# Optimization experiments

Measured on AMD Instinct MI355X. Metric: run time of the kernel, lower is better.

## Reference

```python
import jax, jax.numpy as jnp
import numpy as np

B, T, C = 64, 256, 1024
H, DH = 16, 64           # n_heads, head_dim (C == H*DH)
NP, WS = 16, 2           # n_patches per side, window_size (T == NP*NP)
EPS = 1e-5


def setup_inputs() -> dict:
    key = jax.random.key(0)
    ks = jax.random.split(key, 8)
    s = lambda k, shape, fan: jax.random.normal(k, shape, jnp.float32) * (fan ** -0.5)
    return dict(
        x=jax.random.normal(ks[0], (B, T, C), jnp.float32),
        ln1_g=jnp.ones((C,), jnp.float32), ln1_b=jnp.zeros((C,), jnp.float32),
        Wq=s(ks[1], (H, C, DH), C), Wk=s(ks[2], (H, C, DH), C), Wv=s(ks[3], (H, C, DH), C),
        Wp=s(ks[4], (C, C), C), bp=jnp.zeros((C,), jnp.float32),
        ln2_g=jnp.ones((C,), jnp.float32), ln2_b=jnp.zeros((C,), jnp.float32),
        W1=s(ks[5], (C, C), C), b1=jnp.zeros((C,), jnp.float32),
        W2=s(ks[6], (C, C), C), b2=jnp.zeros((C,), jnp.float32))


def _ln(x, g, b):
    m = x.mean(-1, keepdims=True)
    v = x.var(-1, keepdims=True)
    return (x - m) * jax.lax.rsqrt(v + EPS) * g + b


def reference(x, ln1_g, ln1_b, Wq, Wk, Wv, Wp, bp, ln2_g, ln2_b, W1, b1, W2, b2):
    h = NP // WS                      # windows per side = 8
    nw = h * h                        # 64 windows of WS*WS = 4 tokens
    xn = _ln(x, ln1_g, ln1_b)
    # window partition: [B, T, C] -> [B*nw, WS*WS, C]
    xw = (xn.reshape(B, h, WS, h, WS, C)
            .transpose(0, 1, 3, 2, 4, 5)
            .reshape(B * nw, WS * WS, C))
    # all-heads batched QKV (original loops over heads; math identical since
    # torch.cat of per-head outputs == head-axis stack then reshape)
    q = jnp.einsum('ntc,hcd->nhtd', xw, Wq)
    k = jnp.einsum('ntc,hcd->nhtd', xw, Wk)
    v = jnp.einsum('ntc,hcd->nhtd', xw, Wv)
    # NOTE: scale is C**-0.5 with C = d_model (faithful to source, not head_dim)
    wei = jax.nn.softmax(jnp.einsum('nhqd,nhkd->nhqk', q, k) * (C ** -0.5), axis=-1)
    att = jnp.einsum('nhqk,nhkd->nhqd', wei, v)
    att = att.transpose(0, 2, 1, 3).reshape(B * nw, WS * WS, C)
    att = att @ Wp + bp
    # residual adds the LayerNorm-ed, window-partitioned x (faithful quirk)
    xr = xw + att
    # reverse window partition -> [B, T, C]
    xr = (xr.reshape(B, h, h, WS, WS, C)
            .transpose(0, 1, 3, 2, 4, 5)
            .reshape(B, T, C))
    ff = jax.nn.gelu(_ln(xr, ln2_g, ln2_b) @ W1 + b1, approximate=False) @ W2 + b2
    return xr + ff
```

## Files before the change

### kernel.cpp

```cpp
#include <hip/hip_runtime.h>
#include <math.h>

typedef unsigned short u16;
typedef unsigned int   u32;

using f32x4  = __attribute__((ext_vector_type(4))) float;
using s16x8  = __attribute__((ext_vector_type(8))) short;
using u16x8  = __attribute__((ext_vector_type(8))) unsigned short;

__device__ __forceinline__ u16 f2b(float f) {
    u32 u = __float_as_uint(f);
    u += 0x7FFFu + ((u >> 16) & 1u);
    return (u16)(u >> 16);
}
__device__ __forceinline__ float b2f(u16 u) { return __uint_as_float(((u32)u) << 16); }

__device__ __forceinline__ int natrow(int R) {
    int b = R >> 8, r8 = R & 255, w = r8 >> 2, t = r8 & 3;
    return (b << 8) + ((((w >> 3) << 1) + (t >> 1)) << 4) + ((w & 7) << 1) + (t & 1);
}

__device__ __forceinline__ void gll16(const void* g, void* l) {
    __builtin_amdgcn_global_load_lds(
        (const __attribute__((address_space(1))) void*)g,
        (__attribute__((address_space(3))) void*)l, 16, 0, 0);
}

__device__ __forceinline__ void transpose_body(
    const float* __restrict__ in, u16* __restrict__ out, int R, int C)
{
    __shared__ float tile[32][33];
    const int tx = threadIdx.x, ty = threadIdx.y;
    const int c  = blockIdx.x * 32 + tx;
    const int r0 = blockIdx.y * 32;
#pragma unroll
    for (int i = 0; i < 32; i += 8) tile[ty + i][tx] = in[(size_t)(r0 + ty + i) * C + c];
    __syncthreads();
    const int orow0 = blockIdx.x * 32;
    const int ocol  = r0 + tx;
#pragma unroll
    for (int i = 0; i < 32; i += 8)
        out[(size_t)(orow0 + ty + i) * R + ocol] = f2b(tile[tx][ty + i]);
}

__global__ __launch_bounds__(256) void transpose_qkv(
    const float* __restrict__ Wq, const float* __restrict__ Wk,
    const float* __restrict__ Wv, u16* __restrict__ out)
{
    const int z = blockIdx.z;
    const float* in = (z < 16 ? Wq : z < 32 ? Wk : Wv) + (size_t)(z & 15) * 65536;
    transpose_body(in, out + (size_t)z * 65536, 1024, 64);
}

__global__ __launch_bounds__(256) void transpose_pw(
    const float* __restrict__ Wp, const float* __restrict__ W1,
    const float* __restrict__ W2, u16* __restrict__ out)
{
    const int z = blockIdx.z;
    const float* in = z == 0 ? Wp : z == 1 ? W1 : W2;
    transpose_body(in, out + (size_t)z * 1048576, 1024, 1024);
}

template<int MAP, int BIN>
__global__ __launch_bounds__(256) void ln_kernel(
    const void* __restrict__ X, const float* __restrict__ g, const float* __restrict__ bta,
    u16* __restrict__ outB)
{
    const int R   = blockIdx.x;
    const int src = MAP ? natrow(R) : R;
    float x0, x1, x2, x3;
    if (BIN) {
        const ushort4 r = ((const ushort4*)((const u16*)X + (size_t)src * 1024))[threadIdx.x];
        x0 = b2f(r.x); x1 = b2f(r.y); x2 = b2f(r.z); x3 = b2f(r.w);
    } else {
        const float4 r = ((const float4*)((const float*)X + (size_t)src * 1024))[threadIdx.x];
        x0 = r.x; x1 = r.y; x2 = r.z; x3 = r.w;
    }
    float s  = x0 + x1 + x2 + x3;
    float s2 = x0 * x0 + x1 * x1 + x2 * x2 + x3 * x3;
#pragma unroll
    for (int o = 32; o; o >>= 1) { s += __shfl_xor(s, o); s2 += __shfl_xor(s2, o); }
    __shared__ float red[8];
    const int w = threadIdx.x >> 6, l = threadIdx.x & 63;
    if (l == 0) { red[w] = s; red[w + 4] = s2; }
    __syncthreads();
    s  = red[0] + red[1] + red[2] + red[3];
    s2 = red[4] + red[5] + red[6] + red[7];
    const float mean = s * (1.f / 1024.f);
    const float var  = s2 * (1.f / 1024.f) - mean * mean;
    const float rinv = rsqrtf(var + 1e-5f);
    const float4 gv = ((const float4*)g)[threadIdx.x];
    const float4 bv = ((const float4*)bta)[threadIdx.x];
    ((ushort4*)(outB + (size_t)R * 1024))[threadIdx.x] = make_ushort4(
        f2b((x0 - mean) * rinv * gv.x + bv.x), f2b((x1 - mean) * rinv * gv.y + bv.y),
        f2b((x2 - mean) * rinv * gv.z + bv.z), f2b((x3 - mean) * rinv * gv.w + bv.w));
}

template<int MODE>
__global__ __launch_bounds__(512, 2) void gemm256(
    const u16* __restrict__ A, const u16* __restrict__ Bt,
    const float* __restrict__ bias, const void* __restrict__ resid,
    void* __restrict__ Out, int M, int N, int K, int LDA, int NB)
{
    extern __shared__ char lds[];
    const int NT = K >> 6;
    const int nblk = gridDim.x;
    const int lb = (blockIdx.x & 7) * (nblk >> 3) + (blockIdx.x >> 3);
    const int mb = lb / NB, nb = lb - mb * NB;
    const int row0 = mb * 256, col0 = nb * 256;
    const int tid = threadIdx.x;
    const int w = tid >> 6, l = tid & 63;
    const int wr = w >> 2, wc = w & 3;
    const int lr = l & 15, kg = l >> 4;
    const int xs = (lr & 7) << 4;
    const int koff[2] = { (kg * 16) ^ xs, (64 + kg * 16) ^ xs };
    const int abase_l = wr * 8192 + lr * 128;
    const int bbase_l = wc * 4096 + lr * 128;

    f32x4 acc[2][2][4][2] = {};
    s16x8 a0[4][2], a1[4][2], b0[2][2], b1[2][2];

    auto stage = [&](int ts, int item) {
        if (ts >= NT) return;
        const int d = ts & 1;
        const int isB = item & 1, h = item >> 1;
        char* lbase = lds + (isB ? 65536 : 0) + d * 32768 + h * 16384;
        const u16* gptr = isB ? Bt : A;
        const int ld = isB ? K : LDA;
        const int blk0 = (isB ? col0 : row0) + h * 128;
#pragma unroll
        for (int j = 0; j < 2; ++j) {
            const int p = j * 512 + tid;
            const int q = p ^ ((p >> 3) & 7);
            const int grow = blk0 + (q >> 3);
            const int gcol = ts * 64 + (q & 7) * 8;
            gll16(gptr + (size_t)grow * ld + gcol, lbase + (j * 8 + w) * 1024);
        }
    };

#define LOAD_A(dst, qm) do { \
    _Pragma("unroll") for (int kk = 0; kk < 2; ++kk) \
    _Pragma("unroll") for (int i = 0; i < 4; ++i) \
        dst[i][kk] = *(const s16x8*)(Ab + (qm) * 16384 + abase_l + i * 2048 + koff[kk]); \
} while (0)
#define LOAD_B(dst, qn) do { \
    _Pragma("unroll") for (int kk = 0; kk < 2; ++kk) \
    _Pragma("unroll") for (int n = 0; n < 2; ++n) \
        dst[n][kk] = *(const s16x8*)(Bb + (qn) * 16384 + bbase_l + n * 2048 + koff[kk]); \
} while (0)
#define MFMA_Q(qm, qn, aa, bb) do { \
    __builtin_amdgcn_s_setprio(1); \
    _Pragma("unroll") for (int kk = 0; kk < 2; ++kk) \
    _Pragma("unroll") for (int i = 0; i < 4; ++i) \
    _Pragma("unroll") for (int n = 0; n < 2; ++n) \
        acc[qm][qn][i][n] = __builtin_amdgcn_mfma_f32_16x16x32_bf16( \
            aa[i][kk], bb[n][kk], acc[qm][qn][i][n], 0, 0, 0); \
    __builtin_amdgcn_s_setprio(0); \
    __builtin_amdgcn_sched_barrier(0); \
} while (0)
#define WAIT_LGKM(n) do { \
    asm volatile("s_waitcnt lgkmcnt(" #n ")" ::: "memory"); \
    __builtin_amdgcn_sched_barrier(0); \
} while (0)

    stage(0, 0); stage(0, 1); stage(0, 2); stage(0, 3);
    asm volatile("s_waitcnt vmcnt(0)" ::: "memory");
    __builtin_amdgcn_s_barrier();

    for (int t = 0; t < NT; ++t) {
        const char* Ab = lds + (t & 1) * 32768;
        const char* Bb = lds + 65536 + (t & 1) * 32768;
        LOAD_A(a0, 0); LOAD_B(b0, 0);
        __builtin_amdgcn_sched_barrier(0);
        LOAD_A(a1, 1);
        __builtin_amdgcn_sched_barrier(0);
        LOAD_B(b1, 1);
        __builtin_amdgcn_sched_barrier(0);
        stage(t + 1, 0); stage(t + 1, 1); stage(t + 1, 2); stage(t + 1, 3);
        __builtin_amdgcn_sched_barrier(0);
        WAIT_LGKM(12);
        MFMA_Q(0, 0, a0, b0);
        WAIT_LGKM(4);
        MFMA_Q(1, 0, a1, b0);
        WAIT_LGKM(0);
        MFMA_Q(1, 1, a1, b1);
        MFMA_Q(0, 1, a0, b1);
        if (t < NT - 1) {
            asm volatile("s_waitcnt vmcnt(0)" ::: "memory");
            __builtin_amdgcn_s_barrier();
            __builtin_amdgcn_sched_barrier(0);
        }
    }
#undef LOAD_A
#undef LOAD_B
#undef MFMA_Q
#undef WAIT_LGKM

#pragma unroll
    for (int qm = 0; qm < 2; ++qm)
#pragma unroll
    for (int i = 0; i < 4; ++i) {
        const int grb = row0 + qm * 128 + wr * 64 + i * 16 + kg * 4;
#pragma unroll
        for (int qn = 0; qn < 2; ++qn)
#pragma unroll
        for (int n = 0; n < 2; ++n) {
            const int gc = col0 + qn * 128 + wc * 32 + n * 16 + lr;
#pragma unroll
            for (int j = 0; j < 4; ++j) {
                const int gr = grb + j;
                const float v = acc[qm][qn][i][n][j];
                if (MODE == 0) {
                    ((u16*)Out)[(size_t)gr * N + gc] = f2b(v);
                } else if (MODE == 2) {
                    const float tt = v + bias[gc];
                    ((u16*)Out)[(size_t)gr * N + gc] = f2b(0.5f * tt * (1.f + erff(tt * 0.70710678118f)));
                } else if (MODE == 3) {
                    ((float*)Out)[(size_t)natrow(gr) * N + gc] =
                        v + bias[gc] + b2f(((const u16*)resid)[(size_t)gr * N + gc]);
                } else {
                    ((u16*)Out)[(size_t)gr * N + gc] =
                        f2b(v + bias[gc] + b2f(((const u16*)resid)[(size_t)gr * N + gc]));
                }
            }
        }
    }
}

__global__ __launch_bounds__(256) void attn_kernel(u16* __restrict__ QKV)
{
    const int w = threadIdx.x >> 6, l = threadIdx.x & 63;
    const int n = blockIdx.x * 4 + w;
    u16* base = QKV + (size_t)n * 4 * 3072;
    const float scale = 0.03125f;
#pragma unroll
    for (int c = 0; c < 2; ++c) {
        const int col = c * 512 + l * 8;
        u16x8 qr[4], kr[4], vr[4];
#pragma unroll
        for (int t = 0; t < 4; ++t) {
            qr[t] = *(const u16x8*)(base + t * 3072 + col);
            kr[t] = *(const u16x8*)(base + t * 3072 + 1024 + col);
            vr[t] = *(const u16x8*)(base + t * 3072 + 2048 + col);
        }
        float qf[4][8], kf[4][8];
#pragma unroll
        for (int t = 0; t < 4; ++t)
#pragma unroll
            for (int j = 0; j < 8; ++j) { qf[t][j] = b2f(qr[t][j]); kf[t][j] = b2f(kr[t][j]); }
        float s[4][4];
#pragma unroll
        for (int t = 0; t < 4; ++t)
#pragma unroll
            for (int u = 0; u < 4; ++u) {
                float p = qf[t][0] * kf[u][0];
#pragma unroll
                for (int j = 1; j < 8; ++j) p += qf[t][j] * kf[u][j];
                p += __shfl_xor(p, 1); p += __shfl_xor(p, 2); p += __shfl_xor(p, 4);
                s[t][u] = p * scale;
            }
#pragma unroll
        for (int t = 0; t < 4; ++t) {
            const float m = fmaxf(fmaxf(s[t][0], s[t][1]), fmaxf(s[t][2], s[t][3]));
            const float e0 = expf(s[t][0] - m), e1 = expf(s[t][1] - m);
            const float e2 = expf(s[t][2] - m), e3 = expf(s[t][3] - m);
            const float inv = 1.f / (e0 + e1 + e2 + e3);
            u16x8 o;
#pragma unroll
            for (int j = 0; j < 8; ++j)
                o[j] = f2b((e0 * b2f(vr[0][j]) + e1 * b2f(vr[1][j]) +
                            e2 * b2f(vr[2][j]) + e3 * b2f(vr[3][j])) * inv);
            *(u16x8*)(base + t * 3072 + col) = o;
        }
    }
}

extern "C" void kernel_launch(void* const* d_in, const int* in_sizes, int n_in,
                              void* d_out, int out_size, void* d_ws, size_t ws_size,
                              hipStream_t stream)
{
    const float* x    = (const float*)d_in[0];
    const float* ln1g = (const float*)d_in[1];
    const float* ln1b = (const float*)d_in[2];
    const float* Wq   = (const float*)d_in[3];
    const float* Wk   = (const float*)d_in[4];
    const float* Wv   = (const float*)d_in[5];
    const float* Wp   = (const float*)d_in[6];
    const float* bp   = (const float*)d_in[7];
    const float* ln2g = (const float*)d_in[8];
    const float* ln2b = (const float*)d_in[9];
    const float* W1   = (const float*)d_in[10];
    const float* b1   = (const float*)d_in[11];
    const float* W2   = (const float*)d_in[12];
    const float* b2   = (const float*)d_in[13];
    float* out = (float*)d_out;

    char* ws = (char*)d_ws;
    const size_t MB = 1024 * 1024;
    u16* xr_b  = (u16*)ws;
    u16* xw_b  = (u16*)(ws + 32 * MB);
    u16* qkv   = (u16*)(ws + 64 * MB);
    u16* h1b   = (u16*)(ws + 64 * MB);
    u16* ln2bf = (u16*)(ws + 160 * MB);
    u16* WqkvT = (u16*)(ws + 192 * MB);
    u16* WpT   = (u16*)(ws + 198 * MB);
    u16* W1T   = WpT + (1u << 20);
    u16* W2T   = W1T + (1u << 20);

    hipFuncSetAttribute((const void*)gemm256<0>, hipFuncAttributeMaxDynamicSharedMemorySize, 131072);
    hipFuncSetAttribute((const void*)gemm256<2>, hipFuncAttributeMaxDynamicSharedMemorySize, 131072);
    hipFuncSetAttribute((const void*)gemm256<3>, hipFuncAttributeMaxDynamicSharedMemorySize, 131072);
    hipFuncSetAttribute((const void*)gemm256<5>, hipFuncAttributeMaxDynamicSharedMemorySize, 131072);

    const int M = 16384, K = 1024;
    dim3 tpb(32, 8);
    transpose_qkv<<<dim3(2, 32, 48), tpb, 0, stream>>>(Wq, Wk, Wv, WqkvT);
    transpose_pw <<<dim3(32, 32, 3), tpb, 0, stream>>>(Wp, W1, W2, WpT);

    ln_kernel<1, 0><<<16384, 256, 0, stream>>>(x, ln1g, ln1b, xw_b);

    gemm256<0><<<768, 512, 131072, stream>>>(xw_b, WqkvT, nullptr, nullptr, qkv, M, 3072, K, K, 12);

    attn_kernel<<<1024, 256, 0, stream>>>(qkv);

    gemm256<5><<<256, 512, 131072, stream>>>(qkv, WpT, bp, xw_b, xr_b, M, 1024, K, 3072, 4);

    ln_kernel<0, 1><<<16384, 256, 0, stream>>>(xr_b, ln2g, ln2b, ln2bf);

    gemm256<2><<<256, 512, 131072, stream>>>(ln2bf, W1T, b1, nullptr, h1b, M, 1024, K, K, 4);

    gemm256<3><<<256, 512, 131072, stream>>>(h1b, W2T, b2, xr_b, out, M, 1024, K, K, 4);
}
```

Baseline: 312.8 us.

## Replace 256x256 GEMM tiles with 128x256 tiles using K=32 steps and 4 waves

Rewrites the bf16 GEMM kernel to use a 128x256 output tile with 256 threads, a 32-wide K step, and a 48KB double-buffered LDS layout, instead of a 256x256 tile with 512 threads and 128KB LDS. This doubles the grid size, which should give better wave balance across CUs on MI355X and allow more resident blocks per CU. In exchange, arithmetic intensity per tile is lower, each tile makes more global-to-LDS load passes, and there are twice as many barriers per unit of K. The global source pointers are precomputed once per thread, and the LDS swizzle is changed to fit the narrower K slab.

New measurement: 334.8 us. 7.1% more time.

```diff
diff --git a/kernel.cpp b/kernel.cpp
--- a/kernel.cpp
+++ b/kernel.cpp
@@ -97,119 +97,108 @@
 }
 
 template<int MODE>
-__global__ __launch_bounds__(512, 2) void gemm256(
+__global__ __launch_bounds__(256, 2) void gemm128(
     const u16* __restrict__ A, const u16* __restrict__ Bt,
     const float* __restrict__ bias, const void* __restrict__ resid,
     void* __restrict__ Out, int M, int N, int K, int LDA, int NB)
 {
     extern __shared__ char lds[];
-    const int NT = K >> 6;
+    const int NT = K >> 5;
     const int nblk = gridDim.x;
     const int lb = (blockIdx.x & 7) * (nblk >> 3) + (blockIdx.x >> 3);
     const int mb = lb / NB, nb = lb - mb * NB;
-    const int row0 = mb * 256, col0 = nb * 256;
+    const int row0 = mb * 128, col0 = nb * 256;
     const int tid = threadIdx.x;
     const int w = tid >> 6, l = tid & 63;
-    const int wr = w >> 2, wc = w & 3;
     const int lr = l & 15, kg = l >> 4;
-    const int xs = (lr & 7) << 4;
-    const int koff[2] = { (kg * 16) ^ xs, (64 + kg * 16) ^ xs };
-    const int abase_l = wr * 8192 + lr * 128;
-    const int bbase_l = wc * 4096 + lr * 128;
-
-    f32x4 acc[2][2][4][2] = {};
-    s16x8 a0[4][2], a1[4][2], b0[2][2], b1[2][2];
-
-    auto stage = [&](int ts, int item) {
-        if (ts >= NT) return;
-        const int d = ts & 1;
-        const int isB = item & 1, h = item >> 1;
-        char* lbase = lds + (isB ? 65536 : 0) + d * 32768 + h * 16384;
-        const u16* gptr = isB ? Bt : A;
-        const int ld = isB ? K : LDA;
-        const int blk0 = (isB ? col0 : row0) + h * 128;
-#pragma unroll
-        for (int j = 0; j < 2; ++j) {
-            const int p = j * 512 + tid;
-            const int q = p ^ ((p >> 3) & 7);
-            const int grow = blk0 + (q >> 3);
-            const int gcol = ts * 64 + (q & 7) * 8;
-            gll16(gptr + (size_t)grow * ld + gcol, lbase + (j * 8 + w) * 1024);
-        }
-    };
-
-#define LOAD_A(dst, qm) do { \
-    _Pragma("unroll") for (int kk = 0; kk < 2; ++kk) \
-    _Pragma("unroll") for (int i = 0; i < 4; ++i) \
-        dst[i][kk] = *(const s16x8*)(Ab + (qm) * 16384 + abase_l + i * 2048 + koff[kk]); \
+    const int laneoff = (lr >> 1) * 128 +
+        ((((lr & 1) << 6) | (kg << 4)) ^ (((lr >> 1) & 7) << 4));
+    const char* vA = lds + laneoff;
+    const char* vB = lds + 8192 + w * 4096 + laneoff;
+
+    const u16* sA[2]; const u16* sB[4];
+#pragma unroll
+    for (int j = 0; j < 2; ++j) {
+        const int c = j * 256 + tid, rp = c >> 3, sl = (c & 7) ^ (rp & 7);
+        sA[j] = A + (size_t)(row0 + rp * 2 + (sl >> 2)) * LDA + (sl & 3) * 8;
+    }
+#pragma unroll
+    for (int j = 0; j < 4; ++j) {
+        const int c = j * 256 + tid, rp = c >> 3, sl = (c & 7) ^ (rp & 7);
+        sB[j] = Bt + (size_t)(col0 + rp * 2 + (sl >> 2)) * K + (sl & 3) * 8;
+    }
+
+    f32x4 acc[8][4] = {};
+    s16x8 a[8], b[4];
+
+#define SB __builtin_amdgcn_sched_barrier(0)
+#define STAGE(dd, ts) do { \
+    gll16(sA[0] + (ts) * 32, lds + (dd) * 24576 +         w * 1024); \
+    gll16(sA[1] + (ts) * 32, lds + (dd) * 24576 +  4096 + w * 1024); \
+    gll16(sB[0] + (ts) * 32, lds + (dd) * 24576 +  8192 + w * 1024); \
+    gll16(sB[1] + (ts) * 32, lds + (dd) * 24576 + 12288 + w * 1024); \
+    gll16(sB[2] + (ts) * 32, lds + (dd) * 24576 + 16384 + w * 1024); \
+    gll16(sB[3] + (ts) * 32, lds + (dd) * 24576 + 20480 + w * 1024); \
 } while (0)
-#define LOAD_B(dst, qn) do { \
-    _Pragma("unroll") for (int kk = 0; kk < 2; ++kk) \
-    _Pragma("unroll") for (int n = 0; n < 2; ++n) \
-        dst[n][kk] = *(const s16x8*)(Bb + (qn) * 16384 + bbase_l + n * 2048 + koff[kk]); \
+#define G4(i) do { \
+    acc[i][0] = __builtin_amdgcn_mfma_f32_16x16x32_bf16(a[i], b[0], acc[i][0], 0, 0, 0); \
+    acc[i][1] = __builtin_amdgcn_mfma_f32_16x16x32_bf16(a[i], b[1], acc[i][1], 0, 0, 0); \
+    acc[i][2] = __builtin_amdgcn_mfma_f32_16x16x32_bf16(a[i], b[2], acc[i][2], 0, 0, 0); \
+    acc[i][3] = __builtin_amdgcn_mfma_f32_16x16x32_bf16(a[i], b[3], acc[i][3], 0, 0, 0); \
 } while (0)
-#define MFMA_Q(qm, qn, aa, bb) do { \
+#define TILE(d, t) do { \
+    b[0] = *(const s16x8*)(vB + (d) * 24576 +    0); \
+    b[1] = *(const s16x8*)(vB + (d) * 24576 + 1024); \
+    b[2] = *(const s16x8*)(vB + (d) * 24576 + 2048); \
+    b[3] = *(const s16x8*)(vB + (d) * 24576 + 3072); \
+    SB; \
+    a[0] = *(const s16x8*)(vA + (d) * 24576 +    0); \
+    a[1] = *(const s16x8*)(vA + (d) * 24576 + 1024); \
+    a[2] = *(const s16x8*)(vA + (d) * 24576 + 2048); \
+    a[3] = *(const s16x8*)(vA + (d) * 24576 + 3072); \
+    SB; \
+    a[4] = *(const s16x8*)(vA + (d) * 24576 + 4096); \
+    a[5] = *(const s16x8*)(vA + (d) * 24576 + 5120); \
+    a[6] = *(const s16x8*)(vA + (d) * 24576 + 6144); \
+    a[7] = *(const s16x8*)(vA + (d) * 24576 + 7168); \
+    SB; \
+    if ((t) + 1 < NT) STAGE((d) ^ 1, (t) + 1); \
+    SB; \
     __builtin_amdgcn_s_setprio(1); \
-    _Pragma("unroll") for (int kk = 0; kk < 2; ++kk) \
-    _Pragma("unroll") for (int i = 0; i < 4; ++i) \
-    _Pragma("unroll") for (int n = 0; n < 2; ++n) \
-        acc[qm][qn][i][n] = __builtin_amdgcn_mfma_f32_16x16x32_bf16( \
-            aa[i][kk], bb[n][kk], acc[qm][qn][i][n], 0, 0, 0); \
-    __builtin_amdgcn_s_setprio(0); \
-    __builtin_amdgcn_sched_barrier(0); \
+    asm volatile("s_waitcnt lgkmcnt(4)" ::: "memory"); SB; \
+    G4(0); G4(1); G4(2); G4(3); \
+    asm volatile("s_waitcnt lgkmcnt(0)" ::: "memory"); SB; \
+    G4(4); G4(5); G4(6); G4(7); \
+    __builtin_amdgcn_s_setprio(0); SB; \
+    if ((t) + 1 < NT) { \
+        asm volatile("s_waitcnt vmcnt(0)" ::: "memory"); \
+        __builtin_amdgcn_s_barrier(); SB; \
+    } \
 } while (0)
-#define WAIT_LGKM(n) do { \
-    asm volatile("s_waitcnt lgkmcnt(" #n ")" ::: "memory"); \
-    __builtin_amdgcn_sched_barrier(0); \
-} while (0)
-
-    stage(0, 0); stage(0, 1); stage(0, 2); stage(0, 3);
+
+    STAGE(0, 0);
     asm volatile("s_waitcnt vmcnt(0)" ::: "memory");
     __builtin_amdgcn_s_barrier();
 
-    for (int t = 0; t < NT; ++t) {
-        const char* Ab = lds + (t & 1) * 32768;
-        const char* Bb = lds + 65536 + (t & 1) * 32768;
-        LOAD_A(a0, 0); LOAD_B(b0, 0);
-        __builtin_amdgcn_sched_barrier(0);
-        LOAD_A(a1, 1);
-        __builtin_amdgcn_sched_barrier(0);
-        LOAD_B(b1, 1);
-        __builtin_amdgcn_sched_barrier(0);
-        stage(t + 1, 0); stage(t + 1, 1); stage(t + 1, 2); stage(t + 1, 3);
-        __builtin_amdgcn_sched_barrier(0);
-        WAIT_LGKM(12);
-        MFMA_Q(0, 0, a0, b0);
-        WAIT_LGKM(4);
-        MFMA_Q(1, 0, a1, b0);
-        WAIT_LGKM(0);
-        MFMA_Q(1, 1, a1, b1);
-        MFMA_Q(0, 1, a0, b1);
-        if (t < NT - 1) {
-            asm volatile("s_waitcnt vmcnt(0)" ::: "memory");
-            __builtin_amdgcn_s_barrier();
-            __builtin_amdgcn_sched_barrier(0);
-        }
-    }
-#undef LOAD_A
-#undef LOAD_B
-#undef MFMA_Q
-#undef WAIT_LGKM
-
-#pragma unroll
-    for (int qm = 0; qm < 2; ++qm)
-#pragma unroll
-    for (int i = 0; i < 4; ++i) {
-        const int grb = row0 + qm * 128 + wr * 64 + i * 16 + kg * 4;
-#pragma unroll
-        for (int qn = 0; qn < 2; ++qn)
-#pragma unroll
-        for (int n = 0; n < 2; ++n) {
-            const int gc = col0 + qn * 128 + wc * 32 + n * 16 + lr;
+    for (int t = 0; t < NT; t += 2) {
+        TILE(0, t);
+        TILE(1, t + 1);
+    }
+#undef SB
+#undef STAGE
+#undef G4
+#undef TILE
+
+#pragma unroll
+    for (int i = 0; i < 8; ++i) {
+        const int grb = row0 + i * 16 + kg * 4;
+#pragma unroll
+        for (int n = 0; n < 4; ++n) {
+            const int gc = col0 + w * 64 + n * 16 + lr;
 #pragma unroll
             for (int j = 0; j < 4; ++j) {
                 const int gr = grb + j;
-                const float v = acc[qm][qn][i][n][j];
+                const float v = acc[i][n][j];
                 if (MODE == 0) {
                     ((u16*)Out)[(size_t)gr * N + gc] = f2b(v);
                 } else if (MODE == 2) {
@@ -307,10 +296,10 @@
     u16* W1T   = WpT + (1u << 20);
     u16* W2T   = W1T + (1u << 20);
 
-    hipFuncSetAttribute((const void*)gemm256<0>, hipFuncAttributeMaxDynamicSharedMemorySize, 131072);
-    hipFuncSetAttribute((const void*)gemm256<2>, hipFuncAttributeMaxDynamicSharedMemorySize, 131072);
-    hipFuncSetAttribute((const void*)gemm256<3>, hipFuncAttributeMaxDynamicSharedMemorySize, 131072);
-    hipFuncSetAttribute((const void*)gemm256<5>, hipFuncAttributeMaxDynamicSharedMemorySize, 131072);
+    hipFuncSetAttribute((const void*)gemm128<0>, hipFuncAttributeMaxDynamicSharedMemorySize, 49152);
+    hipFuncSetAttribute((const void*)gemm128<2>, hipFuncAttributeMaxDynamicSharedMemorySize, 49152);
+    hipFuncSetAttribute((const void*)gemm128<3>, hipFuncAttributeMaxDynamicSharedMemorySize, 49152);
+    hipFuncSetAttribute((const void*)gemm128<5>, hipFuncAttributeMaxDynamicSharedMemorySize, 49152);
 
     const int M = 16384, K = 1024;
     dim3 tpb(32, 8);
@@ -319,15 +308,15 @@
 
     ln_kernel<1, 0><<<16384, 256, 0, stream>>>(x, ln1g, ln1b, xw_b);
 
-    gemm256<0><<<768, 512, 131072, stream>>>(xw_b, WqkvT, nullptr, nullptr, qkv, M, 3072, K, K, 12);
+    gemm128<0><<<1536, 256, 49152, stream>>>(xw_b, WqkvT, nullptr, nullptr, qkv, M, 3072, K, K, 12);
 
     attn_kernel<<<1024, 256, 0, stream>>>(qkv);
 
-    gemm256<5><<<256, 512, 131072, stream>>>(qkv, WpT, bp, xw_b, xr_b, M, 1024, K, 3072, 4);
+    gemm128<5><<<512, 256, 49152, stream>>>(qkv, WpT, bp, xw_b, xr_b, M, 1024, K, 3072, 4);
 
     ln_kernel<0, 1><<<16384, 256, 0, stream>>>(xr_b, ln2g, ln2b, ln2bf);
 
-    gemm256<2><<<256, 512, 131072, stream>>>(ln2bf, W1T, b1, nullptr, h1b, M, 1024, K, K, 4);
-
-    gemm256<3><<<256, 512, 131072, stream>>>(h1b, W2T, b2, xr_b, out, M, 1024, K, K, 4);
-}
+    gemm128<2><<<512, 256, 49152, stream>>>(ln2bf, W1T, b1, nullptr, h1b, M, 1024, K, K, 4);
+
+    gemm128<3><<<512, 256, 49152, stream>>>(h1b, W2T, b2, xr_b, out, M, 1024, K, K, 4);
+}
```

## Interleave per-quarter global-to-LDS staging with MFMA phases using partial vmcnt gates

Applied to the files above, without the earlier changes.

Rewrites the GEMM main loop so the four global-to-LDS stage loads for the next K-tile are spread across the four MFMA quarter-phases instead of being issued together. Each phase is guarded by a partial vmcnt wait plus a workgroup barrier, so a quarter can be consumed as soon as its own loads land rather than after the whole tile arrives. The last iteration is peeled so the wait counts can drain to zero. This aims to overlap memory latency with MFMA work more finely, but it adds three more barriers per iteration and relies on exact counter arithmetic.

Measured after the change: 311.0 us. Within noise of the previous version (-0.6%).

```diff
diff --git a/kernel.cpp b/kernel.cpp
--- a/kernel.cpp
+++ b/kernel.cpp
@@ -138,6 +138,7 @@
         }
     };
 
+#define SB __builtin_amdgcn_sched_barrier(0)
 #define LOAD_A(dst, qm) do { \
     _Pragma("unroll") for (int kk = 0; kk < 2; ++kk) \
     _Pragma("unroll") for (int i = 0; i < 4; ++i) \
@@ -147,6 +148,9 @@
     _Pragma("unroll") for (int kk = 0; kk < 2; ++kk) \
     _Pragma("unroll") for (int n = 0; n < 2; ++n) \
         dst[n][kk] = *(const s16x8*)(Bb + (qn) * 16384 + bbase_l + n * 2048 + koff[kk]); \
+} while (0)
+#define LGKM0 do { \
+    asm volatile("s_waitcnt lgkmcnt(0)" ::: "memory"); SB; \
 } while (0)
 #define MFMA_Q(qm, qn, aa, bb) do { \
     __builtin_amdgcn_s_setprio(1); \
@@ -155,46 +159,60 @@
     _Pragma("unroll") for (int n = 0; n < 2; ++n) \
         acc[qm][qn][i][n] = __builtin_amdgcn_mfma_f32_16x16x32_bf16( \
             aa[i][kk], bb[n][kk], acc[qm][qn][i][n], 0, 0, 0); \
-    __builtin_amdgcn_s_setprio(0); \
-    __builtin_amdgcn_sched_barrier(0); \
-} while (0)
-#define WAIT_LGKM(n) do { \
-    asm volatile("s_waitcnt lgkmcnt(" #n ")" ::: "memory"); \
-    __builtin_amdgcn_sched_barrier(0); \
+    __builtin_amdgcn_s_setprio(0); SB; \
+} while (0)
+#define GATE(NSTR) do { \
+    asm volatile("s_waitcnt vmcnt(" NSTR ")" ::: "memory"); \
+    __builtin_amdgcn_s_barrier(); SB; \
 } while (0)
 
     stage(0, 0); stage(0, 1); stage(0, 2); stage(0, 3);
-    asm volatile("s_waitcnt vmcnt(0)" ::: "memory");
-    __builtin_amdgcn_s_barrier();
-
-    for (int t = 0; t < NT; ++t) {
+
+    for (int t = 0; t < NT - 1; ++t) {
         const char* Ab = lds + (t & 1) * 32768;
         const char* Bb = lds + 65536 + (t & 1) * 32768;
-        LOAD_A(a0, 0); LOAD_B(b0, 0);
-        __builtin_amdgcn_sched_barrier(0);
-        LOAD_A(a1, 1);
-        __builtin_amdgcn_sched_barrier(0);
-        LOAD_B(b1, 1);
-        __builtin_amdgcn_sched_barrier(0);
-        stage(t + 1, 0); stage(t + 1, 1); stage(t + 1, 2); stage(t + 1, 3);
-        __builtin_amdgcn_sched_barrier(0);
-        WAIT_LGKM(12);
+        GATE("4");
+        LOAD_A(a0, 0); LOAD_B(b0, 0); SB;
+        stage(t + 1, 0); SB;
+        LGKM0;
         MFMA_Q(0, 0, a0, b0);
-        WAIT_LGKM(4);
+        GATE("4");
+        LOAD_A(a1, 1); SB;
+        stage(t + 1, 1); SB;
+        LGKM0;
         MFMA_Q(1, 0, a1, b0);
-        WAIT_LGKM(0);
+        GATE("4");
+        LOAD_B(b1, 1); SB;
+        stage(t + 1, 2); SB;
+        LGKM0;
+        MFMA_Q(1, 1, a1, b1);
+        stage(t + 1, 3); SB;
+        MFMA_Q(0, 1, a0, b1);
+    }
+    {
+        const int t = NT - 1;
+        const char* Ab = lds + (t & 1) * 32768;
+        const char* Bb = lds + 65536 + (t & 1) * 32768;
+        GATE("4");
+        LOAD_A(a0, 0); LOAD_B(b0, 0); SB;
+        LGKM0;
+        MFMA_Q(0, 0, a0, b0);
+        GATE("2");
+        LOAD_A(a1, 1); SB;
+        LGKM0;
+        MFMA_Q(1, 0, a1, b0);
+        GATE("0");
+        LOAD_B(b1, 1); SB;
+        LGKM0;
         MFMA_Q(1, 1, a1, b1);
         MFMA_Q(0, 1, a0, b1);
-        if (t < NT - 1) {
-            asm volatile("s_waitcnt vmcnt(0)" ::: "memory");
-            __builtin_amdgcn_s_barrier();
-            __builtin_amdgcn_sched_barrier(0);
-        }
-    }
+    }
+#undef SB
 #undef LOAD_A
 #undef LOAD_B
+#undef LGKM0
 #undef MFMA_Q
-#undef WAIT_LGKM
+#undef GATE
 
 #pragma unroll
     for (int qm = 0; qm < 2; ++qm)
```
